# Kernel tuning notes

Hardware: AMD Instinct MI355X
Metric: run time of the kernel (lower is better)

## Reference

```python
import jax, jax.numpy as jnp
import numpy as np

MEM_DIM = 4096
FEATURE_DIM = 1024
BATCH = 16384
EPS = 1e-12


def setup_inputs() -> dict:
    key = jax.random.key(0)
    k_z, k_mem = jax.random.split(key)
    z = jax.random.normal(k_z, (BATCH, FEATURE_DIM), dtype=jnp.float32)
    # torch reset_parameters: uniform(-stdv, stdv) with stdv = 1/sqrt(feature_dim)
    stdv = 1.0 / np.sqrt(FEATURE_DIM)
    memory = jax.random.uniform(k_mem, (MEM_DIM, FEATURE_DIM), dtype=jnp.float32,
                                minval=-stdv, maxval=stdv)
    return {"z": z, "memory": memory}


def hard_shrink_relu(w, lambd, eps=EPS):
    # relu(w - lambd) * w / (|w - lambd| + eps)
    d = w - lambd
    return jax.nn.relu(d) * w / (jnp.abs(d) + eps)


def reference(z, memory):
    # w: [B, M] attention scores over memory slots
    w = jnp.matmul(z, memory.T)
    w = jax.nn.softmax(w, axis=1)
    lambd = 2.0 / w.shape[1]  # default lambd = 2/N with N = mem_dim
    w_hat = hard_shrink_relu(w, lambd)
    att = jax.nn.softmax(w_hat, axis=1)
    z_hat = jnp.matmul(att, memory)  # [B, C]
    return (att, z_hat)
```

## Files before the change

kernel.cpp:

```cpp
#include <hip/hip_runtime.h>
#include <stdint.h>

#define BATCH   16384
#define MEM_DIM 4096
#define FEAT    1024
#define LAMBD   0.00048828125f
#define SEPS    1e-12f

typedef __attribute__((ext_vector_type(8))) short short8;
typedef __attribute__((ext_vector_type(4))) float f32x4;

__device__ __forceinline__ unsigned short f2bf(float x) {
  uint32_t u = __builtin_bit_cast(uint32_t, x);
  u += 0x7fffu + ((u >> 16) & 1u);
  return (unsigned short)(u >> 16);
}
__device__ __forceinline__ float bf2f(unsigned short b) {
  uint32_t u = ((uint32_t)b) << 16;
  return __builtin_bit_cast(float, u);
}

__global__ __launch_bounds__(256) void prep_kernel(
    const float* __restrict__ z, const float* __restrict__ mem,
    unsigned short* __restrict__ zb, unsigned short* __restrict__ memb,
    unsigned short* __restrict__ membT) {
  const int b = blockIdx.x;
  if (b < 8192) {
    size_t i = ((size_t)b * 256 + threadIdx.x) * 8;
    f32x4 a = __builtin_nontemporal_load((const f32x4*)(z + i));
    f32x4 c = __builtin_nontemporal_load((const f32x4*)(z + i + 4));
    union { unsigned short u[8]; short8 v; } r;
    r.u[0] = f2bf(a.x); r.u[1] = f2bf(a.y); r.u[2] = f2bf(a.z); r.u[3] = f2bf(a.w);
    r.u[4] = f2bf(c.x); r.u[5] = f2bf(c.y); r.u[6] = f2bf(c.z); r.u[7] = f2bf(c.w);
    *(short8*)(zb + i) = r.v;
  } else {
    __shared__ unsigned short tile[32][33];
    const int bb = b - 8192;
    const int mt = bb & 127;
    const int ct = bb >> 7;
    const int tx = threadIdx.x & 31;
    const int ty = threadIdx.x >> 5;
    #pragma unroll
    for (int r = ty; r < 32; r += 8) {
      const unsigned short bf =
          f2bf(__builtin_nontemporal_load(mem + (size_t)(mt * 32 + r) * FEAT + ct * 32 + tx));
      tile[r][tx] = bf;
      memb[(size_t)(mt * 32 + r) * FEAT + ct * 32 + tx] = bf;
    }
    __syncthreads();
    #pragma unroll
    for (int r = ty; r < 32; r += 8)
      membT[(size_t)(ct * 32 + r) * MEM_DIM + mt * 32 + tx] = tile[tx][r];
  }
}


#define LDSB(db, ab, h) ((((db)*2 + (ab))*2 + (h)) * 16384)

#define CFENCE asm volatile("" ::: "memory")
#define BAR()  do { CFENCE; __builtin_amdgcn_s_barrier(); CFENCE; } while (0)
#define LGKM0  asm volatile("s_waitcnt lgkmcnt(0)" ::: "memory")
#define LGKM8  asm volatile("s_waitcnt lgkmcnt(8)" ::: "memory")
#define VM4    asm volatile("s_waitcnt vmcnt(4)" ::: "memory")

#define STAGE(src, base, h, db, ab, kb) do {                                        \
    __builtin_amdgcn_global_load_lds(                                               \
      (const __attribute__((address_space(1))) uint32_t*)((src) + (base) +          \
          (size_t)(h) * 128 * KC + rel0 + (kb)),                                    \
      (__attribute__((address_space(3))) uint32_t*)(lds + LDSB(db, ab, h) + tid*16),\
      16, 0, 0);                                                                    \
    __builtin_amdgcn_global_load_lds(                                               \
      (const __attribute__((address_space(1))) uint32_t*)((src) + (base) +          \
          (size_t)(h) * 128 * KC + rel1 + (kb)),                                    \
      (__attribute__((address_space(3))) uint32_t*)(lds + LDSB(db, ab, h) + 8192 +  \
          tid*16),                                                                  \
      16, 0, 0);                                                                    \
  } while (0)

#define RD_A(db, mh)                                                                \
  _Pragma("unroll") for (int mi = 0; mi < 4; ++mi) {                                \
    _Pragma("unroll") for (int kk = 0; kk < 2; ++kk)                                \
      af[mi][kk] = *(const short8*)(aP##db + ((mh) << 13) + (mi << 11) + (kk << 10)); \
  }

#define RD_B2(db, n0)                                                               \
  _Pragma("unroll") for (int ni = 0; ni < 2; ++ni) {                                \
    _Pragma("unroll") for (int kk = 0; kk < 2; ++kk)                                \
      bfr[(n0) + ni][kk] = *(const short8*)(bP##db + (((n0) + ni) << 11) + (kk << 10)); \
  }

#define MFMA_Q(mh, nh) do {                                                         \
    __builtin_amdgcn_s_setprio(1);                                                  \
    _Pragma("unroll") for (int mi = 0; mi < 4; ++mi)                                \
    _Pragma("unroll") for (int ni = 0; ni < 2; ++ni)                                \
    _Pragma("unroll") for (int kk = 0; kk < 2; ++kk)                                \
      acc[(mh)*4 + mi][(nh)*2 + ni] = __builtin_amdgcn_mfma_f32_16x16x32_bf16(      \
          af[mi][kk], bfr[(nh)*2 + ni][kk], acc[(mh)*4 + mi][(nh)*2 + ni], 0, 0, 0);\
    __builtin_amdgcn_s_setprio(0);                                                  \
  } while (0)

template<bool OUT_BF16, int KC, int CHAIN, int NBN>
__global__ __launch_bounds__(512, 2)
void gemm256(const unsigned short* __restrict__ A, const unsigned short* __restrict__ Bt,
             float* __restrict__ Cf, unsigned short* __restrict__ Cb, const int ldc)
{
  constexpr int NT = KC / 64;
  constexpr int LOG2NT = (NT == 16) ? 4 : 6;
  constexpr int HNIT = NT / 2;

  __shared__ __align__(16) char lds[131072];

  const int tid  = threadIdx.x;
  const int lane = tid & 63;
  const int wid  = tid >> 6;
  const int wm = wid >> 2;
  const int wn = wid & 3;
  const int lrow = lane & 15;
  const int lkg  = lane >> 4;

  int bm0, bn;
  if constexpr (CHAIN == 4) {
    const int bid = (int)blockIdx.x;
    const int xcd = bid & 7;
    const int t   = bid >> 3;
    const int ghi = t >> 4;
    bn = t & 15;
    const int grp = ghi * 8 + xcd;
    bm0 = grp * 4;
  } else {
    const int nwg = (int)gridDim.x;
    int wg = (int)blockIdx.x;
    wg = (wg & 7) * (nwg >> 3) + (wg >> 3);
    bm0 = wg / NBN;
    bn  = wg % NBN;
  }

  size_t rel0, rel1;
  {
    #pragma unroll
    for (int j = 0; j < 2; ++j) {
      const int c = j * 512 + tid;
      const int d = c * 16;
      const int s = d >> 10;
      int w = d & 1023;
      w ^= ((w >> 9) & 1) << 5;
      const int row  = ((s >> 1) << 4) + (w >> 6);
      const int colE = ((s & 1) << 5) + ((w & 63) >> 1);
      const size_t r = (size_t)row * KC + colE;
      if (j == 0) rel0 = r; else rel1 = r;
    }
  }
  const size_t baseA0 = (size_t)bm0 * 256 * KC;
  const size_t segStep = (size_t)256 * KC;
  const size_t baseB = (size_t)bn * 256 * KC;

  auto baseAOf = [&](int g) {
    int s = g >> LOG2NT;
    if (s >= CHAIN) s = CHAIN - 1;
    return baseA0 + (size_t)s * segStep;
  };
  auto kbOf = [&](int g) { return (g & (NT - 1)) * 64; };

  const int lane_base = (((lrow << 6) | (lkg << 4)) ^ ((((lrow >> 3) & 1)) << 5));
  const char* aP0 = lds + LDSB(0, 0, 0) + wm * 16384 + lane_base;
  const char* aP1 = lds + LDSB(1, 0, 0) + wm * 16384 + lane_base;
  const char* bP0 = lds + LDSB(0, 1, 0) + (wn >> 1) * 16384 + ((wn & 1) << 13) + lane_base;
  const char* bP1 = lds + LDSB(1, 1, 0) + (wn >> 1) * 16384 + ((wn & 1) << 13) + lane_base;

  f32x4 acc[8][4] = {};
  short8 af[4][2], bfr[4][2];

  STAGE(A,  baseA0, 0, 0, 0, 0);
  STAGE(A,  baseA0, 1, 0, 0, 0);
  STAGE(Bt, baseB, 0, 0, 1, 0);
  STAGE(Bt, baseB, 1, 0, 1, 0);
  STAGE(Bt, baseB, 0, 1, 1, 64);
  STAGE(Bt, baseB, 1, 1, 1, 64);
  VM4;
  BAR();

  #pragma unroll 1
  for (int git = 0; git < CHAIN * HNIT; ++git) {
    const int g1 = 2 * git + 1, g2 = 2 * git + 2, g3 = 2 * git + 3;
    const size_t bA1 = baseAOf(g1), bA2 = baseAOf(g2);
    const int kb1 = kbOf(g1), kb2 = kbOf(g2), kb3 = kbOf(g3);

    RD_A(0, 0); RD_B2(0, 0);
    STAGE(A, bA1, 0, 1, 0, kb1);
    LGKM8;
    BAR(); LGKM0; MFMA_Q(0, 0); BAR();
    RD_B2(0, 2);
    STAGE(A, bA1, 1, 1, 0, kb1);
    BAR(); LGKM0; MFMA_Q(0, 1); BAR();
    RD_A(0, 1);
    STAGE(Bt, baseB, 0, 0, 1, kb2);
    BAR(); LGKM0; MFMA_Q(1, 0); BAR();
    STAGE(Bt, baseB, 1, 0, 1, kb2);
    BAR(); LGKM0; MFMA_Q(1, 1); VM4; BAR();

    RD_A(1, 0); RD_B2(1, 0);
    STAGE(A, bA2, 0, 0, 0, kb2);
    LGKM8;
    BAR(); LGKM0; MFMA_Q(0, 0); BAR();
    RD_B2(1, 2);
    STAGE(A, bA2, 1, 0, 0, kb2);
    BAR(); LGKM0; MFMA_Q(0, 1); BAR();
    RD_A(1, 1);
    STAGE(Bt, baseB, 0, 1, 1, kb3);
    BAR(); LGKM0; MFMA_Q(1, 0); BAR();
    STAGE(Bt, baseB, 1, 1, 1, kb3);
    BAR(); LGKM0; MFMA_Q(1, 1); VM4; BAR();

    if (((git + 1) & (HNIT - 1)) == 0) {
      const int s = ((git + 1) >> (LOG2NT - 1)) - 1;
      const int row0 = (bm0 + s) * 256 + wm * 128 + lkg * 4;
      const int col0 = bn * 256 + wn * 64 + lrow;
      #pragma unroll
      for (int mi = 0; mi < 8; ++mi)
        #pragma unroll
        for (int ni = 0; ni < 4; ++ni) {
          #pragma unroll
          for (int r = 0; r < 4; ++r) {
            const size_t row = row0 + mi * 16 + r;
            const int col = col0 + ni * 16;
            if (OUT_BF16) Cb[row * ldc + col] = f2bf(acc[mi][ni][r]);
            else          Cf[row * ldc + col] = acc[mi][ni][r];
          }
          acc[mi][ni] = (f32x4){0.f, 0.f, 0.f, 0.f};
        }
    }
  }
}

__global__ __launch_bounds__(256, 4)
void softmax_shrink_kernel(const unsigned short* __restrict__ W,
                           float* __restrict__ att,
                           unsigned short* __restrict__ attb)
{
  const int lane = threadIdx.x & 63;
  const int row  = blockIdx.x * 4 + (threadIdx.x >> 6);
  const unsigned short* wr = W + (size_t)row * MEM_DIM;

  float v[64];
  #pragma unroll
  for (int c = 0; c < 8; ++c) {
    union { short8 s; unsigned short u[8]; } x;
    x.s = __builtin_nontemporal_load((const short8*)(wr + c * 512 + lane * 8));
    #pragma unroll
    for (int j = 0; j < 8; ++j) v[c * 8 + j] = bf2f(x.u[j]);
  }

  float m0 = v[0], m1 = v[1], m2 = v[2], m3 = v[3];
  #pragma unroll
  for (int j = 4; j < 64; j += 4) {
    m0 = fmaxf(m0, v[j]); m1 = fmaxf(m1, v[j + 1]);
    m2 = fmaxf(m2, v[j + 2]); m3 = fmaxf(m3, v[j + 3]);
  }
  float m = fmaxf(fmaxf(m0, m1), fmaxf(m2, m3));
  #pragma unroll
  for (int o = 32; o > 0; o >>= 1) m = fmaxf(m, __shfl_xor(m, o, 64));

  float s0 = 0.f, s1 = 0.f, s2 = 0.f, s3 = 0.f;
  #pragma unroll
  for (int j = 0; j < 64; j += 4) {
    v[j]     = __expf(v[j]     - m); s0 += v[j];
    v[j + 1] = __expf(v[j + 1] - m); s1 += v[j + 1];
    v[j + 2] = __expf(v[j + 2] - m); s2 += v[j + 2];
    v[j + 3] = __expf(v[j + 3] - m); s3 += v[j + 3];
  }
  float s = (s0 + s1) + (s2 + s3);
  #pragma unroll
  for (int o = 32; o > 0; o >>= 1) s += __shfl_xor(s, o, 64);
  const float inv1 = 1.f / s;

  #pragma unroll
  for (int j = 0; j < 64; ++j) {
    const float p = v[j] * inv1;
    const float d = p - LAMBD;
    v[j] = (d > 0.f) ? (d * p / (d + SEPS)) : 0.f;
  }

  m0 = v[0]; m1 = v[1]; m2 = v[2]; m3 = v[3];
  #pragma unroll
  for (int j = 4; j < 64; j += 4) {
    m0 = fmaxf(m0, v[j]); m1 = fmaxf(m1, v[j + 1]);
    m2 = fmaxf(m2, v[j + 2]); m3 = fmaxf(m3, v[j + 3]);
  }
  float mm = fmaxf(fmaxf(m0, m1), fmaxf(m2, m3));
  #pragma unroll
  for (int o = 32; o > 0; o >>= 1) mm = fmaxf(mm, __shfl_xor(mm, o, 64));

  s0 = s1 = s2 = s3 = 0.f;
  #pragma unroll
  for (int j = 0; j < 64; j += 4) {
    v[j]     = __expf(v[j]     - mm); s0 += v[j];
    v[j + 1] = __expf(v[j + 1] - mm); s1 += v[j + 1];
    v[j + 2] = __expf(v[j + 2] - mm); s2 += v[j + 2];
    v[j + 3] = __expf(v[j + 3] - mm); s3 += v[j + 3];
  }
  s = (s0 + s1) + (s2 + s3);
  #pragma unroll
  for (int o = 32; o > 0; o >>= 1) s += __shfl_xor(s, o, 64);
  const float inv2 = 1.f / s;

  #pragma unroll
  for (int j = 0; j < 64; ++j) v[j] *= inv2;

  float* arow = att + (size_t)row * MEM_DIM;
  #pragma unroll
  for (int c = 0; c < 8; ++c) {
    const int base = c * 512 + lane * 8;
    f32x4 o0 = {v[c*8],     v[c*8+1], v[c*8+2], v[c*8+3]};
    f32x4 o1 = {v[c*8+4],   v[c*8+5], v[c*8+6], v[c*8+7]};
    *(f32x4*)(arow + base)     = o0;
    *(f32x4*)(arow + base + 4) = o1;
  }
  unsigned short* ab = attb + (size_t)row * MEM_DIM;
  #pragma unroll
  for (int c = 0; c < 8; ++c) {
    const int base = c * 512 + lane * 8;
    union { short8 s; unsigned short u[8]; } r;
    #pragma unroll
    for (int j = 0; j < 8; ++j) r.u[j] = f2bf(v[c*8 + j]);
    *(short8*)(ab + base) = r.s;
  }
}

extern "C" void kernel_launch(void* const* d_in, const int* in_sizes, int n_in,
                              void* d_out, int out_size, void* d_ws, size_t ws_size,
                              hipStream_t stream) {
  const float* z   = (const float*)d_in[0];
  const float* mem = (const float*)d_in[1];
  float* att_out  = (float*)d_out;
  float* zhat_out = (float*)d_out + (size_t)BATCH * MEM_DIM;

  unsigned short* zb    = (unsigned short*)d_ws;
  unsigned short* memb  = zb + (size_t)BATCH * FEAT;
  unsigned short* membT = memb + (size_t)MEM_DIM * FEAT;
  unsigned short* wbuf  = membT + (size_t)FEAT * MEM_DIM;

  prep_kernel<<<8192 + 4096, 256, 0, stream>>>(z, mem, zb, memb, membT);

  gemm256<true, FEAT, 4, 16><<<256, 512, 0, stream>>>(zb, memb, nullptr, wbuf, MEM_DIM);

  softmax_shrink_kernel<<<BATCH / 4, 256, 0, stream>>>(wbuf, att_out, wbuf);

  gemm256<false, MEM_DIM, 1, 4><<<256, 512, 0, stream>>>(wbuf, membT, zhat_out, nullptr, FEAT);
}
```

Measured before the change: 360.5 us.

## Replace chained persistent M-tile loop with one-tile-per-block GEMM launch

The first GEMM no longer walks four consecutive M-tiles per workgroup with a continuous K pipeline across tile boundaries. Instead it launches one workgroup per 256x256 output tile, so there are four times as many blocks and the epilogue is written once after the K loop. This simplifies indexing and raises the number of resident blocks, but gives up reusing the resident B tile and the cross-tile prefetch overlap, and adds per-block prologue cost.

```diff
diff --git a/kernel.cpp b/kernel.cpp
--- a/kernel.cpp
+++ b/kernel.cpp
@@ -99,13 +99,12 @@
     __builtin_amdgcn_s_setprio(0);                                                  \
   } while (0)
 
-template<bool OUT_BF16, int KC, int CHAIN, int NBN>
+template<bool OUT_BF16, int KC, int NBN>
 __global__ __launch_bounds__(512, 2)
 void gemm256(const unsigned short* __restrict__ A, const unsigned short* __restrict__ Bt,
              float* __restrict__ Cf, unsigned short* __restrict__ Cb, const int ldc)
 {
   constexpr int NT = KC / 64;
-  constexpr int LOG2NT = (NT == 16) ? 4 : 6;
   constexpr int HNIT = NT / 2;
 
   __shared__ __align__(16) char lds[131072];
@@ -118,22 +117,11 @@
   const int lrow = lane & 15;
   const int lkg  = lane >> 4;
 
-  int bm0, bn;
-  if constexpr (CHAIN == 4) {
-    const int bid = (int)blockIdx.x;
-    const int xcd = bid & 7;
-    const int t   = bid >> 3;
-    const int ghi = t >> 4;
-    bn = t & 15;
-    const int grp = ghi * 8 + xcd;
-    bm0 = grp * 4;
-  } else {
-    const int nwg = (int)gridDim.x;
-    int wg = (int)blockIdx.x;
-    wg = (wg & 7) * (nwg >> 3) + (wg >> 3);
-    bm0 = wg / NBN;
-    bn  = wg % NBN;
-  }
+  const int nwg = (int)gridDim.x;
+  int wg = (int)blockIdx.x;
+  wg = (wg & 7) * (nwg >> 3) + (wg >> 3);
+  const int bm = wg / NBN;
+  const int bn = wg % NBN;
 
   size_t rel0, rel1;
   {
@@ -150,15 +138,9 @@
       if (j == 0) rel0 = r; else rel1 = r;
     }
   }
-  const size_t baseA0 = (size_t)bm0 * 256 * KC;
-  const size_t segStep = (size_t)256 * KC;
+  const size_t baseA = (size_t)bm * 256 * KC;
   const size_t baseB = (size_t)bn * 256 * KC;
 
-  auto baseAOf = [&](int g) {
-    int s = g >> LOG2NT;
-    if (s >= CHAIN) s = CHAIN - 1;
-    return baseA0 + (size_t)s * segStep;
-  };
   auto kbOf = [&](int g) { return (g & (NT - 1)) * 64; };
 
   const int lane_base = (((lrow << 6) | (lkg << 4)) ^ ((((lrow >> 3) & 1)) << 5));
@@ -170,8 +152,8 @@
   f32x4 acc[8][4] = {};
   short8 af[4][2], bfr[4][2];
 
-  STAGE(A,  baseA0, 0, 0, 0, 0);
-  STAGE(A,  baseA0, 1, 0, 0, 0);
+  STAGE(A,  baseA, 0, 0, 0, 0);
+  STAGE(A,  baseA, 1, 0, 0, 0);
   STAGE(Bt, baseB, 0, 0, 1, 0);
   STAGE(Bt, baseB, 1, 0, 1, 0);
   STAGE(Bt, baseB, 0, 1, 1, 64);
@@ -180,17 +162,17 @@
   BAR();
 
   #pragma unroll 1
-  for (int git = 0; git < CHAIN * HNIT; ++git) {
-    const int g1 = 2 * git + 1, g2 = 2 * git + 2, g3 = 2 * git + 3;
-    const size_t bA1 = baseAOf(g1), bA2 = baseAOf(g2);
-    const int kb1 = kbOf(g1), kb2 = kbOf(g2), kb3 = kbOf(g3);
+  for (int git = 0; git < HNIT; ++git) {
+    const int kb1 = kbOf(2 * git + 1);
+    const int kb2 = kbOf(2 * git + 2);
+    const int kb3 = kbOf(2 * git + 3);
 
     RD_A(0, 0); RD_B2(0, 0);
-    STAGE(A, bA1, 0, 1, 0, kb1);
+    STAGE(A, baseA, 0, 1, 0, kb1);
     LGKM8;
     BAR(); LGKM0; MFMA_Q(0, 0); BAR();
     RD_B2(0, 2);
-    STAGE(A, bA1, 1, 1, 0, kb1);
+    STAGE(A, baseA, 1, 1, 0, kb1);
     BAR(); LGKM0; MFMA_Q(0, 1); BAR();
     RD_A(0, 1);
     STAGE(Bt, baseB, 0, 0, 1, kb2);
@@ -199,37 +181,32 @@
     BAR(); LGKM0; MFMA_Q(1, 1); VM4; BAR();
 
     RD_A(1, 0); RD_B2(1, 0);
-    STAGE(A, bA2, 0, 0, 0, kb2);
+    STAGE(A, baseA, 0, 0, 0, kb2);
     LGKM8;
     BAR(); LGKM0; MFMA_Q(0, 0); BAR();
     RD_B2(1, 2);
-    STAGE(A, bA2, 1, 0, 0, kb2);
+    STAGE(A, baseA, 1, 0, 0, kb2);
     BAR(); LGKM0; MFMA_Q(0, 1); BAR();
     RD_A(1, 1);
     STAGE(Bt, baseB, 0, 1, 1, kb3);
     BAR(); LGKM0; MFMA_Q(1, 0); BAR();
     STAGE(Bt, baseB, 1, 1, 1, kb3);
     BAR(); LGKM0; MFMA_Q(1, 1); VM4; BAR();
-
-    if (((git + 1) & (HNIT - 1)) == 0) {
-      const int s = ((git + 1) >> (LOG2NT - 1)) - 1;
-      const int row0 = (bm0 + s) * 256 + wm * 128 + lkg * 4;
-      const int col0 = bn * 256 + wn * 64 + lrow;
+  }
+
+  const int row0 = bm * 256 + wm * 128 + lkg * 4;
+  const int col0 = bn * 256 + wn * 64 + lrow;
+  #pragma unroll
+  for (int mi = 0; mi < 8; ++mi)
+    #pragma unroll
+    for (int ni = 0; ni < 4; ++ni)
       #pragma unroll
-      for (int mi = 0; mi < 8; ++mi)
-        #pragma unroll
-        for (int ni = 0; ni < 4; ++ni) {
-          #pragma unroll
-          for (int r = 0; r < 4; ++r) {
-            const size_t row = row0 + mi * 16 + r;
-            const int col = col0 + ni * 16;
-            if (OUT_BF16) Cb[row * ldc + col] = f2bf(acc[mi][ni][r]);
-            else          Cf[row * ldc + col] = acc[mi][ni][r];
-          }
-          acc[mi][ni] = (f32x4){0.f, 0.f, 0.f, 0.f};
-        }
-    }
-  }
+      for (int r = 0; r < 4; ++r) {
+        const size_t row = row0 + mi * 16 + r;
+        const int col = col0 + ni * 16;
+        if (OUT_BF16) Cb[row * ldc + col] = f2bf(acc[mi][ni][r]);
+        else          Cf[row * ldc + col] = acc[mi][ni][r];
+      }
 }
 
 __global__ __launch_bounds__(256, 4)
@@ -341,9 +318,11 @@
 
   prep_kernel<<<8192 + 4096, 256, 0, stream>>>(z, mem, zb, memb, membT);
 
-  gemm256<true, FEAT, 4, 16><<<256, 512, 0, stream>>>(zb, memb, nullptr, wbuf, MEM_DIM);
+  gemm256<true, FEAT, 16><<<(MEM_DIM / 256) * (BATCH / 256), 512, 0, stream>>>(
+      zb, memb, nullptr, wbuf, MEM_DIM);
 
   softmax_shrink_kernel<<<BATCH / 4, 256, 0, stream>>>(wbuf, att_out, wbuf);
 
-  gemm256<false, MEM_DIM, 1, 4><<<256, 512, 0, stream>>>(wbuf, membT, zhat_out, nullptr, FEAT);
-}
+  gemm256<false, MEM_DIM, 4><<<(FEAT / 256) * (BATCH / 256), 512, 0, stream>>>(
+      wbuf, membT, zhat_out, nullptr, FEAT);
+}
```

After: 364.1 us. No clear change (+1.0%).
